# Kernel optimization log

Measured on AMD Instinct MI355X. Metric: run time of the kernel, lower is better.

Reference implementation:

```python
import jax, jax.numpy as jnp
import numpy as np

N_TOKEN = 64
H = 16
D = 1024
D_K = 64
D_V = 64
S3 = 30  # 3 * S, number of gated leading positions
GATE_INIT = 10.0


def setup_inputs() -> dict:
    key = jax.random.key(0)
    ks = jax.random.split(key, 8)
    B, L = 32, 2048
    x = jax.random.normal(ks[0], (B, L, D), dtype=jnp.float32)
    q_init = (1.0 / D_K) ** 0.5
    q_tok = jax.random.uniform(ks[1], (1, N_TOKEN, D), minval=-q_init, maxval=q_init, dtype=jnp.float32)
    scale = 0.02
    Wq = jax.random.normal(ks[2], (D, H * D_K), dtype=jnp.float32) * scale
    Wk = jax.random.normal(ks[3], (D, H * D_K), dtype=jnp.float32) * scale
    Wv = jax.random.normal(ks[4], (D, H * D_V), dtype=jnp.float32) * scale
    Wfc = jax.random.normal(ks[5], (H * D_V, D), dtype=jnp.float32) * scale
    gate_logit = -jnp.ones((S3,), dtype=jnp.float32) * GATE_INIT  # matches module init
    gamma = jnp.ones((D,), dtype=jnp.float32)
    beta = jnp.zeros((D,), dtype=jnp.float32)
    return {"x": x, "q_tok": q_tok, "Wq": Wq, "Wk": Wk, "Wv": Wv, "Wfc": Wfc,
            "gate_logit": gate_logit, "gamma": gamma, "beta": beta}


def reference(x, q_tok, Wq, Wk, Wv, Wfc, gate_logit, gamma, beta):
    # x: [B, L, D]; q_tok: [1, n_token, D]. Dropout is identity (eval mode).
    B, L, _ = x.shape
    temp = D_K ** 0.5

    # Cumulative-product gate over the first 30 positions (the torch for-loop).
    gate = jnp.cumprod(1.0 - jax.nn.sigmoid(gate_logit))  # [30]
    x1 = x.at[:, :S3].multiply(gate[None, :, None])

    q = (q_tok @ Wq).reshape(N_TOKEN, H, D_K)          # [n, H, dk]
    k = (x @ Wk).reshape(B, L, H, D_K)                  # [B, L, H, dk]
    v = (x1 @ Wv).reshape(B, L, H, D_V)                 # [B, L, H, dv]

    scores = jnp.einsum('nhd,blhd->bhnl', q / temp, k)  # [B, H, n, L]
    attn = jax.nn.softmax(scores, axis=-1)
    out = jnp.einsum('bhnl,blhd->bnhd', attn, v).reshape(B, N_TOKEN, H * D_V)

    out = out @ Wfc + q_tok                              # residual with query tokens

    # LayerNorm over last dim, eps=1e-6
    mu = jnp.mean(out, axis=-1, keepdims=True)
    var = jnp.mean(jnp.square(out - mu), axis=-1, keepdims=True)
    out = (out - mu) * jax.lax.rsqrt(var + 1e-6) * gamma + beta
    return out
```

## Files before the change

### kernel.cpp

```cpp
#include <hip/hip_runtime.h>
#include <stdint.h>

typedef unsigned short u16;
typedef short bf16x8 __attribute__((ext_vector_type(8)));
typedef float f32x4 __attribute__((ext_vector_type(4)));

__device__ __forceinline__ u16 f2b(float f) {
  uint32_t u = __builtin_bit_cast(uint32_t, f);
  u += 0x7fffu + ((u >> 16) & 1u);
  return (u16)(u >> 16);
}

__device__ __forceinline__ void gload_lds16(const void* g, void* l) {
  __builtin_amdgcn_global_load_lds(
      (const __attribute__((address_space(1))) void*)g,
      (__attribute__((address_space(3))) void*)l, 16, 0, 0);
}

__global__ void gate_kernel(const float* __restrict__ gl, float* __restrict__ gate) {
  if (threadIdx.x == 0 && blockIdx.x == 0) {
    float g = 1.0f;
    for (int i = 0; i < 30; ++i) {
      float s = 1.0f / (1.0f + __expf(-gl[i]));
      g *= (1.0f - s);
      gate[i] = g;
    }
  }
}

__global__ __launch_bounds__(256) void cvt_kernel(const float* __restrict__ src,
                                                  u16* __restrict__ dst) {
  int64_t i = ((int64_t)blockIdx.x * 256 + threadIdx.x) * 8;
  float4 a = *(const float4*)(src + i);
  float4 b = *(const float4*)(src + i + 4);
  union { u16 u[8]; bf16x8 v; } o;
  o.u[0] = f2b(a.x); o.u[1] = f2b(a.y); o.u[2] = f2b(a.z); o.u[3] = f2b(a.w);
  o.u[4] = f2b(b.x); o.u[5] = f2b(b.y); o.u[6] = f2b(b.z); o.u[7] = f2b(b.w);
  *(bf16x8*)(dst + i) = o.v;
}

__global__ __launch_bounds__(256) void transpose_w_kernel(const float* __restrict__ src,
                                                          u16* __restrict__ dst) {
  __shared__ float ls[64][65];
  int t = threadIdx.x;
  int bx = blockIdx.x & 15;
  int by = blockIdx.x >> 4;
  int r0 = by * 64, c0 = bx * 64;
  int tr = t >> 6, tc = t & 63;
#pragma unroll
  for (int i = 0; i < 16; ++i)
    ls[tr + i * 4][tc] = src[(int64_t)(r0 + tr + i * 4) * 1024 + c0 + tc];
  __syncthreads();
#pragma unroll
  for (int i = 0; i < 16; ++i)
    dst[(int64_t)(c0 + tr + i * 4) * 1024 + r0 + tc] = f2b(ls[tc][tr + i * 4]);
}

__global__ __launch_bounds__(256, 4) void q_gemm_kernel(
    const u16* __restrict__ qtokb, const u16* __restrict__ wqT, u16* __restrict__ qb) {
  __shared__ u16 As[4096];
  __shared__ u16 Bs[8192];
  int n0 = blockIdx.x * 128;
  int t = threadIdx.x, w = t >> 6, lane = t & 63;
  int wn = w * 32;
  f32x4 acc[2][4] = {};
  int l3 = lane >> 3;
  int colE = ((lane & 7) ^ l3) * 8;
  const u16* aS = qtokb + (int64_t)(w * 16 + l3) * 1024 + colE;
  const u16* bS = wqT + (int64_t)(n0 + w * 32 + l3) * 1024 + colE;
  u16* aD = As + w * 1024;
  u16* bD = Bs + w * 2048;
  int l15 = lane & 15, g16 = lane >> 4;
  for (int kt = 0; kt < 16; ++kt) {
    int ko = kt * 64;
    __syncthreads();
    gload_lds16(aS + ko, aD);
    gload_lds16(aS + ko + 8192, aD + 512);
#pragma unroll
    for (int g = 0; g < 4; ++g) gload_lds16(bS + ko + g * 8192, bD + g * 512);
    __syncthreads();
#pragma unroll
    for (int kk = 0; kk < 2; ++kk) {
      int sl = ((kk * 4 + g16) ^ (l15 & 7)) * 8;
      bf16x8 af[4], bf[2];
#pragma unroll
      for (int j = 0; j < 4; ++j) af[j] = *(const bf16x8*)(As + (j * 16 + l15) * 64 + sl);
#pragma unroll
      for (int i = 0; i < 2; ++i) bf[i] = *(const bf16x8*)(Bs + (wn + i * 16 + l15) * 64 + sl);
#pragma unroll
      for (int i = 0; i < 2; ++i)
#pragma unroll
        for (int j = 0; j < 4; ++j)
          acc[i][j] = __builtin_amdgcn_mfma_f32_16x16x32_bf16(bf[i], af[j], acc[i][j], 0, 0, 0);
    }
  }
  const float sc = 1.44269504f / 8.0f;
  int lr = g16 * 4;
#pragma unroll
  for (int i = 0; i < 2; ++i) {
    int colg = n0 + wn + i * 16 + lr;
#pragma unroll
    for (int j = 0; j < 4; ++j) {
      int qrow = j * 16 + l15;
      u16 p[4];
#pragma unroll
      for (int r = 0; r < 4; ++r) p[r] = f2b(acc[i][j][r] * sc);
      *(uint64_t*)(qb + qrow * 1024 + colg) = *(uint64_t*)p;
    }
  }
}

__global__ __launch_bounds__(256, 2) void kv_gemm_kernel(
    const u16* __restrict__ xb, const u16* __restrict__ wkvT,
    const float* __restrict__ gate, u16* __restrict__ kbuf, u16* __restrict__ vT) {
  __shared__ u16 As[8192];
  __shared__ u16 Bs[8192];
  int d = blockIdx.x;
  int x = d & 7;
  int nb = (d >> 3) & 15;
  int mb = (d >> 7) * 8 + x;
  int m0 = mb * 128, n0 = nb * 128;
  int t = threadIdx.x, w = t >> 6, lane = t & 63;
  int wm = (w >> 1) * 64, wn = (w & 1) * 64;
  bool isV = (n0 >= 1024);
  f32x4 acc[4][4] = {};
  int l3 = lane >> 3;
  int colE = ((lane & 7) ^ l3) * 8;
  const u16* aS = xb + (int64_t)(m0 + w * 32 + l3) * 1024 + colE;
  const u16* bS = wkvT + (int64_t)(n0 + w * 32 + l3) * 1024 + colE;
  u16* aD = As + w * 2048;
  u16* bD = Bs + w * 2048;
  int l15 = lane & 15, g16 = lane >> 4;
  for (int kt = 0; kt < 16; ++kt) {
    int ko = kt * 64;
    __syncthreads();
#pragma unroll
    for (int g = 0; g < 4; ++g) {
      gload_lds16(aS + ko + g * 8192, aD + g * 512);
      gload_lds16(bS + ko + g * 8192, bD + g * 512);
    }
    __syncthreads();
#pragma unroll
    for (int kk = 0; kk < 2; ++kk) {
      int sl = ((kk * 4 + g16) ^ (l15 & 7)) * 8;
      bf16x8 af[4], bf[4];
#pragma unroll
      for (int i = 0; i < 4; ++i) af[i] = *(const bf16x8*)(As + (wm + i * 16 + l15) * 64 + sl);
#pragma unroll
      for (int j = 0; j < 4; ++j) bf[j] = *(const bf16x8*)(Bs + (wn + j * 16 + l15) * 64 + sl);
      if (!isV) {
#pragma unroll
        for (int i = 0; i < 4; ++i)
#pragma unroll
          for (int j = 0; j < 4; ++j)
            acc[i][j] = __builtin_amdgcn_mfma_f32_16x16x32_bf16(bf[i], af[j], acc[i][j], 0, 0, 0);
      } else {
#pragma unroll
        for (int i = 0; i < 4; ++i)
#pragma unroll
          for (int j = 0; j < 4; ++j)
            acc[i][j] = __builtin_amdgcn_mfma_f32_16x16x32_bf16(af[i], bf[j], acc[i][j], 0, 0, 0);
      }
    }
  }
  int b = m0 >> 11, lbase = m0 & 2047;
  int lr = g16 * 4;
  if (!isV) {
#pragma unroll
    for (int i = 0; i < 4; ++i) {
      int dkg = n0 + wn + i * 16 + lr;
      int h = dkg >> 6, dkk = dkg & 63;
#pragma unroll
      for (int j = 0; j < 4; ++j) {
        int l = lbase + wm + j * 16 + l15;
        u16 p[4];
#pragma unroll
        for (int r = 0; r < 4; ++r) p[r] = f2b(acc[i][j][r]);
        *(uint64_t*)(kbuf + ((int64_t)((b * 16 + h) * 2048 + l)) * 64 + dkk) = *(uint64_t*)p;
      }
    }
  } else {
#pragma unroll
    for (int j = 0; j < 4; ++j) {
      int dvg = (n0 - 1024) + wn + j * 16 + l15;
      int h = dvg >> 6, dv = dvg & 63;
#pragma unroll
      for (int i = 0; i < 4; ++i) {
        int lg = lbase + wm + i * 16 + lr;
        u16 p[4];
#pragma unroll
        for (int r = 0; r < 4; ++r) {
          float val = acc[i][j][r];
          int ll = lg + r;
          if (ll < 30) val *= gate[ll];
          p[r] = f2b(val);
        }
        *(uint64_t*)(vT + ((int64_t)((b * 16 + h) * 64 + dv)) * 2048 + lg) = *(uint64_t*)p;
      }
    }
  }
}

__global__ __launch_bounds__(256) void attn_kernel(
    const u16* __restrict__ qb, const u16* __restrict__ kbuf,
    const u16* __restrict__ vT, float* __restrict__ pO,
    float* __restrict__ pm, float* __restrict__ ps) {
  __shared__ u16 Ps[4096];
  int bid = blockIdx.x;
  int b = bid >> 6, h = (bid >> 2) & 15, c = bid & 3;
  int t = threadIdx.x, w = t >> 6, lane = t & 63;
  int l15 = lane & 15, g16 = lane >> 4, lh8 = g16 * 8;
  bf16x8 qf0 = *(const bf16x8*)(qb + (w * 16 + l15) * 1024 + h * 64 + lh8);
  bf16x8 qf1 = *(const bf16x8*)(qb + (w * 16 + l15) * 1024 + h * 64 + 32 + lh8);
  const u16* kB = kbuf + (int64_t)(b * 16 + h) * (2048 * 64);
  const u16* vB = vT + (int64_t)(b * 16 + h) * (64 * 2048);
  char* PsW = (char*)Ps + w * 2048;
  float m_r[4] = {-1e30f, -1e30f, -1e30f, -1e30f};
  float s_r[4] = {0.f, 0.f, 0.f, 0.f};
  f32x4 O[4] = {};
  for (int lt = 0; lt < 8; ++lt) {
    int l0 = c * 512 + lt * 64;
    f32x4 S[4];
#pragma unroll
    for (int ls = 0; ls < 4; ++ls) {
      const u16* kr = kB + (l0 + ls * 16 + l15) * 64 + lh8;
      bf16x8 k0 = *(const bf16x8*)(kr);
      bf16x8 k1 = *(const bf16x8*)(kr + 32);
      f32x4 s = {};
      s = __builtin_amdgcn_mfma_f32_16x16x32_bf16(qf0, k0, s, 0, 0, 0);
      s = __builtin_amdgcn_mfma_f32_16x16x32_bf16(qf1, k1, s, 0, 0, 0);
      S[ls] = s;
    }
    float scale[4];
#pragma unroll
    for (int r = 0; r < 4; ++r) {
      float tm = fmaxf(fmaxf(S[0][r], S[1][r]), fmaxf(S[2][r], S[3][r]));
#pragma unroll
      for (int msk = 1; msk < 16; msk <<= 1)
        tm = fmaxf(tm, __shfl_xor(tm, msk, 16));
      float mn = fmaxf(m_r[r], tm);
      scale[r] = exp2f(m_r[r] - mn);
      m_r[r] = mn;
    }
#pragma unroll
    for (int ls = 0; ls < 4; ++ls)
#pragma unroll
      for (int r = 0; r < 4; ++r) S[ls][r] = exp2f(S[ls][r] - m_r[r]);
#pragma unroll
    for (int r = 0; r < 4; ++r) {
      float psm = (S[0][r] + S[1][r]) + (S[2][r] + S[3][r]);
      s_r[r] = s_r[r] * scale[r] + psm;
    }
#pragma unroll
    for (int ls = 0; ls < 4; ++ls)
#pragma unroll
      for (int r = 0; r < 4; ++r) {
        int row = g16 * 4 + r;
        int off = (ls * 16 + l15) * 2;
        *(u16*)(PsW + row * 128 + (off ^ ((row & 7) << 4))) = f2b(S[ls][r]);
      }
#pragma unroll
    for (int d = 0; d < 4; ++d)
#pragma unroll
      for (int r = 0; r < 4; ++r) O[d][r] *= scale[r];
    bf16x8 pa0, pa1;
    {
      int off0 = g16 * 16;
      pa0 = *(const bf16x8*)(PsW + l15 * 128 + (off0 ^ ((l15 & 7) << 4)));
      pa1 = *(const bf16x8*)(PsW + l15 * 128 + ((off0 + 64) ^ ((l15 & 7) << 4)));
    }
#pragma unroll
    for (int d = 0; d < 4; ++d) {
      const u16* vr = vB + (d * 16 + l15) * 2048 + l0 + lh8;
      bf16x8 v0 = *(const bf16x8*)(vr);
      bf16x8 v1 = *(const bf16x8*)(vr + 32);
      O[d] = __builtin_amdgcn_mfma_f32_16x16x32_bf16(pa0, v0, O[d], 0, 0, 0);
      O[d] = __builtin_amdgcn_mfma_f32_16x16x32_bf16(pa1, v1, O[d], 0, 0, 0);
    }
  }
#pragma unroll
  for (int r = 0; r < 4; ++r) {
    float s = s_r[r];
#pragma unroll
    for (int msk = 1; msk < 16; msk <<= 1) s += __shfl_xor(s, msk, 16);
    s_r[r] = s;
  }
  int64_t pbase = (int64_t)bid * 4096;
#pragma unroll
  for (int d = 0; d < 4; ++d)
#pragma unroll
    for (int r = 0; r < 4; ++r) {
      int n = w * 16 + g16 * 4 + r;
      pO[pbase + n * 64 + d * 16 + l15] = O[d][r];
    }
  if (l15 == 0) {
#pragma unroll
    for (int r = 0; r < 4; ++r) {
      int n = w * 16 + g16 * 4 + r;
      pm[bid * 64 + n] = m_r[r];
      ps[bid * 64 + n] = s_r[r];
    }
  }
}

__global__ __launch_bounds__(256) void attn_combine_kernel(
    const float* __restrict__ pO, const float* __restrict__ pm,
    const float* __restrict__ ps, u16* __restrict__ attnout) {
  int bh = blockIdx.x;
  int b = bh >> 4, h = bh & 15;
  int t = threadIdx.x;
  int dv = t & 63, grp = t >> 6;
#pragma unroll
  for (int i = 0; i < 16; ++i) {
    int n = grp * 16 + i;
    int base = bh * 256 + n;
    float m0 = pm[base], m1 = pm[base + 64], m2 = pm[base + 128], m3 = pm[base + 192];
    float M = fmaxf(fmaxf(m0, m1), fmaxf(m2, m3));
    float w0 = exp2f(m0 - M), w1 = exp2f(m1 - M), w2 = exp2f(m2 - M), w3 = exp2f(m3 - M);
    float stot = w0 * ps[base] + w1 * ps[base + 64] + w2 * ps[base + 128] + w3 * ps[base + 192];
    float inv = 1.0f / stot;
    int64_t ob = (int64_t)bh * 16384 + n * 64 + dv;
    float o = w0 * pO[ob] + w1 * pO[ob + 4096] + w2 * pO[ob + 8192] + w3 * pO[ob + 12288];
    attnout[((int64_t)(b * 64 + n)) * 1024 + h * 64 + dv] = f2b(o * inv);
  }
}

__global__ __launch_bounds__(256, 4) void fc_gemm_kernel(
    const u16* __restrict__ a, const u16* __restrict__ bT,
    const float* __restrict__ q_tok, float* __restrict__ out) {
  __shared__ u16 As[8192];
  __shared__ u16 Bs[8192];
  int bid = blockIdx.x;
  int mb = bid >> 3, nb = bid & 7;
  int m0 = mb * 128, n0 = nb * 128;
  int t = threadIdx.x, w = t >> 6, lane = t & 63;
  int wm = (w >> 1) * 64, wn = (w & 1) * 64;
  f32x4 acc[4][4] = {};
  int l3 = lane >> 3;
  int colE = ((lane & 7) ^ l3) * 8;
  const u16* aS = a + (int64_t)(m0 + w * 32 + l3) * 1024 + colE;
  const u16* bS = bT + (int64_t)(n0 + w * 32 + l3) * 1024 + colE;
  u16* aD = As + w * 2048;
  u16* bD = Bs + w * 2048;
  int l15 = lane & 15, g16 = lane >> 4;
  for (int kt = 0; kt < 16; ++kt) {
    int ko = kt * 64;
    __syncthreads();
#pragma unroll
    for (int g = 0; g < 4; ++g) {
      gload_lds16(aS + ko + g * 8192, aD + g * 512);
      gload_lds16(bS + ko + g * 8192, bD + g * 512);
    }
    __syncthreads();
#pragma unroll
    for (int kk = 0; kk < 2; ++kk) {
      int sl = ((kk * 4 + g16) ^ (l15 & 7)) * 8;
      bf16x8 af[4], bf[4];
#pragma unroll
      for (int i = 0; i < 4; ++i) af[i] = *(const bf16x8*)(As + (wm + i * 16 + l15) * 64 + sl);
#pragma unroll
      for (int j = 0; j < 4; ++j) bf[j] = *(const bf16x8*)(Bs + (wn + j * 16 + l15) * 64 + sl);
#pragma unroll
      for (int i = 0; i < 4; ++i)
#pragma unroll
        for (int j = 0; j < 4; ++j)
          acc[i][j] = __builtin_amdgcn_mfma_f32_16x16x32_bf16(bf[i], af[j], acc[i][j], 0, 0, 0);
    }
  }
  int lr = g16 * 4;
#pragma unroll
  for (int i = 0; i < 4; ++i) {
    int colg = n0 + wn + i * 16 + lr;
#pragma unroll
    for (int j = 0; j < 4; ++j) {
      int row = m0 + wm + j * 16 + l15;
      float4 res = *(const float4*)(q_tok + (row & 63) * 1024 + colg);
      float4 o;
      o.x = acc[i][j][0] + res.x;
      o.y = acc[i][j][1] + res.y;
      o.z = acc[i][j][2] + res.z;
      o.w = acc[i][j][3] + res.w;
      *(float4*)(out + (int64_t)row * 1024 + colg) = o;
    }
  }
}

__global__ __launch_bounds__(256) void ln_kernel(
    const float* __restrict__ fc, const float* __restrict__ gamma,
    const float* __restrict__ beta, float* __restrict__ out) {
  __shared__ float red[8];
  int row = blockIdx.x, t = threadIdx.x;
  float4 y = *(const float4*)(fc + (int64_t)row * 1024 + t * 4);
  float s = (y.x + y.y) + (y.z + y.w);
  float ss = (y.x * y.x + y.y * y.y) + (y.z * y.z + y.w * y.w);
#pragma unroll
  for (int msk = 1; msk < 64; msk <<= 1) {
    s += __shfl_xor(s, msk, 64);
    ss += __shfl_xor(ss, msk, 64);
  }
  if ((t & 63) == 0) { red[t >> 6] = s; red[4 + (t >> 6)] = ss; }
  __syncthreads();
  s = (red[0] + red[1]) + (red[2] + red[3]);
  ss = (red[4] + red[5]) + (red[6] + red[7]);
  float mu = s * (1.0f / 1024.0f);
  float var = ss * (1.0f / 1024.0f) - mu * mu;
  float rstd = rsqrtf(var + 1e-6f);
  float4 g = *(const float4*)(gamma + t * 4);
  float4 be = *(const float4*)(beta + t * 4);
  float4 o;
  o.x = (y.x - mu) * rstd * g.x + be.x;
  o.y = (y.y - mu) * rstd * g.y + be.y;
  o.z = (y.z - mu) * rstd * g.z + be.z;
  o.w = (y.w - mu) * rstd * g.w + be.w;
  *(float4*)(out + (int64_t)row * 1024 + t * 4) = o;
}

extern "C" void kernel_launch(void* const* d_in, const int* in_sizes, int n_in,
                              void* d_out, int out_size, void* d_ws, size_t ws_size,
                              hipStream_t stream) {
  const float* x     = (const float*)d_in[0];
  const float* q_tok = (const float*)d_in[1];
  const float* Wq    = (const float*)d_in[2];
  const float* Wk    = (const float*)d_in[3];
  const float* Wv    = (const float*)d_in[4];
  const float* Wfc   = (const float*)d_in[5];
  const float* gl    = (const float*)d_in[6];
  const float* gamma = (const float*)d_in[7];
  const float* beta  = (const float*)d_in[8];
  float* out = (float*)d_out;
  char* ws = (char*)d_ws;

  u16*   xb      = (u16*)(ws);
  u16*   kbuf    = (u16*)(ws + 134217728);
  u16*   vT      = (u16*)(ws + 268435456);
  u16*   wkvT    = (u16*)(ws + 402653184);
  u16*   wfcT    = (u16*)(ws + 406847488);
  u16*   wqT     = (u16*)(ws + 408944640);
  u16*   qtokb   = (u16*)(ws + 411041792);
  u16*   qb      = (u16*)(ws + 411172864);
  float* gate    = (float*)(ws + 411303936);
  u16*   attnout = (u16*)(ws + 411304448);
  float* fcout   = (float*)(ws + 415498752);
  float* pO = (float*)(ws);
  float* pm = (float*)(ws + 33554432);
  float* ps = (float*)(ws + 34078720);

  gate_kernel<<<1, 64, 0, stream>>>(gl, gate);
  cvt_kernel<<<32768, 256, 0, stream>>>(x, xb);
  cvt_kernel<<<32, 256, 0, stream>>>(q_tok, qtokb);
  transpose_w_kernel<<<256, 256, 0, stream>>>(Wk, wkvT);
  transpose_w_kernel<<<256, 256, 0, stream>>>(Wv, wkvT + 1024 * 1024);
  transpose_w_kernel<<<256, 256, 0, stream>>>(Wfc, wfcT);
  transpose_w_kernel<<<256, 256, 0, stream>>>(Wq, wqT);
  q_gemm_kernel<<<8, 256, 0, stream>>>(qtokb, wqT, qb);
  kv_gemm_kernel<<<8192, 256, 0, stream>>>(xb, wkvT, gate, kbuf, vT);
  attn_kernel<<<2048, 256, 0, stream>>>(qb, kbuf, vT, pO, pm, ps);
  attn_combine_kernel<<<512, 256, 0, stream>>>(pO, pm, ps, attnout);
  fc_gemm_kernel<<<128, 256, 0, stream>>>(attnout, wfcT, q_tok, fcout);
  ln_kernel<<<2048, 256, 0, stream>>>(fcout, gamma, beta, out);
}
```

Baseline: 680.3 us.

## Double-buffer LDS tiles in KV GEMM with smaller K step

The KV projection GEMM now keeps two LDS buffers and prefetches the next K slice while running MFMAs on the current one, which removes one barrier per iteration. The K tile shrinks from 64 to 32, and the XOR swizzle is changed to match, so LDS use per block stays the same. The gain is overlap of global-to-LDS loads with compute. The cost is twice as many loop iterations, each doing only one MFMA step between barriers. There is also some risk that the single barrier before reusing a buffer does not fully order the asynchronous LDS loads.

```diff
diff --git a/kernel.cpp b/kernel.cpp
--- a/kernel.cpp
+++ b/kernel.cpp
@@ -113,8 +113,8 @@
 __global__ __launch_bounds__(256, 2) void kv_gemm_kernel(
     const u16* __restrict__ xb, const u16* __restrict__ wkvT,
     const float* __restrict__ gate, u16* __restrict__ kbuf, u16* __restrict__ vT) {
-  __shared__ u16 As[8192];
-  __shared__ u16 Bs[8192];
+  __shared__ u16 As[2][4096];
+  __shared__ u16 Bs[2][4096];
   int d = blockIdx.x;
   int x = d & 7;
   int nb = (d >> 3) & 15;
@@ -124,44 +124,54 @@
   int wm = (w >> 1) * 64, wn = (w & 1) * 64;
   bool isV = (n0 >= 1024);
   f32x4 acc[4][4] = {};
-  int l3 = lane >> 3;
-  int colE = ((lane & 7) ^ l3) * 8;
-  const u16* aS = xb + (int64_t)(m0 + w * 32 + l3) * 1024 + colE;
-  const u16* bS = wkvT + (int64_t)(n0 + w * 32 + l3) * 1024 + colE;
-  u16* aD = As + w * 2048;
-  u16* bD = Bs + w * 2048;
+  int srow = w * 32 + (lane >> 2);
+  int scol = ((lane & 3) ^ ((lane >> 2) & 3)) * 8;
+  const u16* aSrc = xb + (int64_t)(m0 + srow) * 1024 + scol;
+  const u16* bSrc = wkvT + (int64_t)(n0 + srow) * 1024 + scol;
   int l15 = lane & 15, g16 = lane >> 4;
-  for (int kt = 0; kt < 16; ++kt) {
-    int ko = kt * 64;
+  gload_lds16(aSrc, As[0] + w * 1024);
+  gload_lds16(aSrc + 16 * 1024, As[0] + w * 1024 + 512);
+  gload_lds16(bSrc, Bs[0] + w * 1024);
+  gload_lds16(bSrc + 16 * 1024, Bs[0] + w * 1024 + 512);
+  __syncthreads();
+  for (int kt = 0; kt < 32; ++kt) {
+    int cur = kt & 1;
+    if (kt < 31) {
+      int ko = (kt + 1) * 32;
+      u16* aD = As[cur ^ 1] + w * 1024;
+      u16* bD = Bs[cur ^ 1] + w * 1024;
+      gload_lds16(aSrc + ko, aD);
+      gload_lds16(aSrc + 16 * 1024 + ko, aD + 512);
+      gload_lds16(bSrc + ko, bD);
+      gload_lds16(bSrc + 16 * 1024 + ko, bD + 512);
+    }
+    const u16* Ab = As[cur];
+    const u16* Bb = Bs[cur];
+    bf16x8 af[4], bf[4];
+#pragma unroll
+    for (int i = 0; i < 4; ++i) {
+      int row = wm + i * 16 + l15;
+      af[i] = *(const bf16x8*)(Ab + row * 32 + ((g16 ^ (row & 3)) * 8));
+    }
+#pragma unroll
+    for (int j = 0; j < 4; ++j) {
+      int row = wn + j * 16 + l15;
+      bf[j] = *(const bf16x8*)(Bb + row * 32 + ((g16 ^ (row & 3)) * 8));
+    }
+    if (!isV) {
+#pragma unroll
+      for (int i = 0; i < 4; ++i)
+#pragma unroll
+        for (int j = 0; j < 4; ++j)
+          acc[i][j] = __builtin_amdgcn_mfma_f32_16x16x32_bf16(bf[i], af[j], acc[i][j], 0, 0, 0);
+    } else {
+#pragma unroll
+      for (int i = 0; i < 4; ++i)
+#pragma unroll
+        for (int j = 0; j < 4; ++j)
+          acc[i][j] = __builtin_amdgcn_mfma_f32_16x16x32_bf16(af[i], bf[j], acc[i][j], 0, 0, 0);
+    }
     __syncthreads();
-#pragma unroll
-    for (int g = 0; g < 4; ++g) {
-      gload_lds16(aS + ko + g * 8192, aD + g * 512);
-      gload_lds16(bS + ko + g * 8192, bD + g * 512);
-    }
-    __syncthreads();
-#pragma unroll
-    for (int kk = 0; kk < 2; ++kk) {
-      int sl = ((kk * 4 + g16) ^ (l15 & 7)) * 8;
-      bf16x8 af[4], bf[4];
-#pragma unroll
-      for (int i = 0; i < 4; ++i) af[i] = *(const bf16x8*)(As + (wm + i * 16 + l15) * 64 + sl);
-#pragma unroll
-      for (int j = 0; j < 4; ++j) bf[j] = *(const bf16x8*)(Bs + (wn + j * 16 + l15) * 64 + sl);
-      if (!isV) {
-#pragma unroll
-        for (int i = 0; i < 4; ++i)
-#pragma unroll
-          for (int j = 0; j < 4; ++j)
-            acc[i][j] = __builtin_amdgcn_mfma_f32_16x16x32_bf16(bf[i], af[j], acc[i][j], 0, 0, 0);
-      } else {
-#pragma unroll
-        for (int i = 0; i < 4; ++i)
-#pragma unroll
-          for (int j = 0; j < 4; ++j)
-            acc[i][j] = __builtin_amdgcn_mfma_f32_16x16x32_bf16(af[i], bf[j], acc[i][j], 0, 0, 0);
-      }
-    }
   }
   int b = m0 >> 11, lbase = m0 & 2047;
   int lr = g16 * 4;
```

Measured after the change: 800.7 us. 1.18x slower.
